# Performance work log

Measured on AMD Instinct MI355X. Metric: run time of the kernel, lower is better.

## Reference

```python
import jax, jax.numpy as jnp
import numpy as np

N, E = 40000, 640000
S_IN, V_IN = 64, 32            # input irreps: 64x0e + 32x1o (dim 160)
S_MID, V_MID = 96, 128         # tp output: (64+32)x0e, (64+32+32)x1o
S_OUT, V_OUT = 96, 32          # gate irreps_in: 64x0e scalars + 32x0e gates + 32x1o gated
R = 64                         # edge scalar (radial basis) dim
FC_HID = 64
W_NUMEL = 64 + 64 + 32 + 32 + 32  # per-edge tp weights ('uvu', v=1): 224
NUM_NEIGHBORS = 16.0


def setup_inputs() -> dict:
    key = jax.random.key(0)
    ks = jax.random.split(key, 13)
    return {
        "node_features": jax.random.normal(ks[0], (N, S_IN + 3 * V_IN), jnp.float32),
        "node_attr": jnp.ones((N, 1), jnp.float32),
        "edge_src": jax.random.randint(ks[1], (E,), 0, N),
        "edge_dst": jax.random.randint(ks[2], (E,), 0, N),
        "edge_attr": jax.random.normal(ks[3], (E, 4), jnp.float32),
        "edge_scalars": jax.random.normal(ks[4], (E, R), jnp.float32),
        "lin1_ws": jax.random.normal(ks[5], (S_IN, S_IN), jnp.float32),
        "lin1_wv": jax.random.normal(ks[6], (V_IN, V_IN), jnp.float32),
        "fc_w1": jax.random.normal(ks[7], (R, FC_HID), jnp.float32),
        "fc_w2": jax.random.normal(ks[8], (FC_HID, W_NUMEL), jnp.float32),
        "sc_ws": jax.random.normal(ks[9], (S_IN, S_OUT), jnp.float32),
        "sc_wv": jax.random.normal(ks[10], (V_IN, V_OUT), jnp.float32),
        "lin2_ws": jax.random.normal(ks[11], (S_MID, S_OUT), jnp.float32),
        "lin2_wv": jax.random.normal(ks[12], (V_MID, V_OUT), jnp.float32),
    }


def _inv(d):
    return 1.0 / jnp.sqrt(jnp.float32(d))


def _forward(node_features, node_attr, edge_attr, edge_scalars,
             lin1_ws, lin1_wv, fc_w1, fc_w2, sc_ws, sc_wv, lin2_ws, lin2_wv,
             edge_src, edge_dst):
    n = node_features.shape[0]
    s = node_features[:, :S_IN]                      # [N,64] 0e
    v = node_features[:, S_IN:].reshape(n, V_IN, 3)  # [N,32,3] 1o
    a = node_attr                                    # [N,1] scalar node attr

    # self-connection: FullyConnectedTensorProduct(input, 1x0e attr, out) == per-irrep linear
    sc_s = (s @ sc_ws) * a * _inv(S_IN)                                    # [N,96]
    sc_v = jnp.einsum('nci,cd->ndi', v, sc_wv) * a[:, :, None] * _inv(V_IN)  # [N,32,3]

    # lin1
    h_s = (s @ lin1_ws) * a * _inv(S_IN)
    h_v = jnp.einsum('nci,cd->ndi', v, lin1_wv) * a[:, :, None] * _inv(V_IN)

    # per-edge tensor-product weights from FC on edge scalars (silu MLP, no bias)
    hid = jax.nn.silu((edge_scalars @ fc_w1) * _inv(R))
    w = (hid @ fc_w2) * _inv(FC_HID)                 # [E,224]
    w1, w2, w3, w4, w5 = jnp.split(w, [64, 128, 160, 192], axis=-1)

    # gather source node features
    es = h_s[edge_src]                               # [E,64]
    ev = h_v[edge_src]                               # [E,32,3]
    e0 = edge_attr[:, :1]                            # [E,1]  0e
    e1 = edge_attr[:, 1:4]                           # [E,3]  1o

    # Clebsch-Gordan tensor product paths ('uvu', per-edge weights)
    m_s1 = w1 * es * e0                                                   # 0e x 0e -> 0e [E,64]
    m_s2 = w4 * jnp.einsum('eci,ei->ec', ev, e1) * _inv(3)                # 1o x 1o -> 0e [E,32]
    m_v1 = (w2 * es)[:, :, None] * e1[:, None, :]                         # 0e x 1o -> 1o [E,64,3]
    m_v2 = w3[:, :, None] * ev * e0[:, :, None]                           # 1o x 0e -> 1o [E,32,3]
    m_v3 = w5[:, :, None] * jnp.cross(ev, e1[:, None, :]) * _inv(2)       # 1o x 1o -> 1o [E,32,3]

    mid_s = jnp.concatenate([m_s1, m_s2], axis=-1)        # [E,96]
    mid_v = jnp.concatenate([m_v1, m_v2, m_v3], axis=1)   # [E,128,3]

    # scatter-sum to destination nodes, normalized by sqrt(num_neighbors)
    inv_nn = 1.0 / jnp.sqrt(jnp.float32(NUM_NEIGHBORS))
    agg_s = jax.ops.segment_sum(mid_s, edge_dst, num_segments=n) * inv_nn
    agg_v = jax.ops.segment_sum(mid_v, edge_dst, num_segments=n) * inv_nn

    # lin2
    o_s = (agg_s @ lin2_ws) * a * _inv(S_MID)                                  # [N,96]
    o_v = jnp.einsum('nci,cd->ndi', agg_v, lin2_wv) * a[:, :, None] * _inv(V_MID)  # [N,32,3]

    pre_s = sc_s + o_s
    pre_v = sc_v + o_v

    # Gate: silu on scalars, sigmoid gates multiply the l=1 features
    scalars = jax.nn.silu(pre_s[:, :64])
    gates = jax.nn.sigmoid(pre_s[:, 64:96])
    gated = gates[:, :, None] * pre_v                 # [N,32,3]
    return jnp.concatenate([scalars, gated.reshape(n, 3 * V_OUT)], axis=-1)  # [N,160]


def reference(node_features, node_attr, edge_src, edge_dst, edge_attr, edge_scalars,
              lin1_ws, lin1_wv, fc_w1, fc_w2, sc_ws, sc_wv, lin2_ws, lin2_wv):
    return _forward(node_features, node_attr, edge_attr, edge_scalars,
                    lin1_ws, lin1_wv, fc_w1, fc_w2, sc_ws, sc_wv, lin2_ws, lin2_wv,
                    edge_src, edge_dst)
```

## Files before the change

kernel.cpp:

```cpp
#include <hip/hip_runtime.h>

constexpr int N_NODES = 40000;
constexpr int N_EDGES = 640000;

constexpr float C_INV8     = 0.125f;
constexpr float C_INV_S32  = 0.17677669529663687f;
constexpr float C_INV_S3   = 0.57735026918962576f;
constexpr float C_INV_S2   = 0.70710678118654752f;
constexpr float C_INV_S96  = 0.10206207261596575f;
constexpr float C_INV_S128 = 0.08838834764831845f;
constexpr float C_INV_NN   = 0.25f;

typedef __attribute__((ext_vector_type(8))) short short8;
typedef __attribute__((ext_vector_type(4))) float f32x4;

__device__ __forceinline__ unsigned short f2bf(float x) {
  __bf16 b = (__bf16)x;
  return __builtin_bit_cast(unsigned short, b);
}
__device__ __forceinline__ float bf2f(unsigned short h) {
  return __uint_as_float(((unsigned int)h) << 16);
}

__global__ __launch_bounds__(256) void k_prep(
    const float* __restrict__ fc_w1, const float* __restrict__ fc_w2,
    const float* __restrict__ lin2_ws, const float* __restrict__ lin2_wv,
    unsigned short* __restrict__ w1t, unsigned short* __restrict__ w2t,
    unsigned short* __restrict__ wst, unsigned short* __restrict__ wvt)
{
  int t = blockIdx.x * 256 + threadIdx.x;
  if (t < 4096) {
    int c = t >> 6, k = t & 63;
    w1t[c * 64 + k] = f2bf(fc_w1[k * 64 + c]);
  } else if (t < 4096 + 14336) {
    int u = t - 4096; int c = u >> 6, k = u & 63;
    w2t[c * 64 + k] = f2bf(fc_w2[k * 224 + c]);
  } else if (t < 18432 + 9216) {
    int u = t - 18432; int c = u / 96, k = u - c * 96;
    wst[c * 96 + k] = f2bf(lin2_ws[k * 96 + c] * (C_INV_NN * C_INV_S96));
  } else if (t < 27648 + 4096) {
    int u = t - 27648; int d = u >> 7, k = u & 127;
    wvt[d * 128 + k] = f2bf(lin2_wv[k * 32 + d] * (C_INV_NN * C_INV_S128));
  }
}

__global__ __launch_bounds__(256) void k_node(
    const float* __restrict__ nf, const float* __restrict__ attr,
    const float* __restrict__ ws_, const float* __restrict__ wv_,
    float* __restrict__ h_s, float* __restrict__ h_v)
{
  int t = blockIdx.x * 256 + threadIdx.x;
  if (t < N_NODES * 64) {
    int n = t >> 6, c = t & 63;
    const float* s = nf + (long)n * 160;
    float acc = 0.f;
    #pragma unroll 8
    for (int k = 0; k < 64; ++k) acc = fmaf(s[k], ws_[k * 64 + c], acc);
    h_s[t] = acc * attr[n] * C_INV8;
  } else {
    int u = t - N_NODES * 64;
    if (u >= N_NODES * 32) return;
    int n = u >> 5, d = u & 31;
    const float* v = nf + (long)n * 160 + 64;
    float a0 = 0.f, a1 = 0.f, a2 = 0.f;
    #pragma unroll 8
    for (int c = 0; c < 32; ++c) {
      float wv = wv_[c * 32 + d];
      a0 = fmaf(v[3 * c + 0], wv, a0);
      a1 = fmaf(v[3 * c + 1], wv, a1);
      a2 = fmaf(v[3 * c + 2], wv, a2);
    }
    float sc = attr[n] * C_INV_S32;
    h_v[(long)u * 3 + 0] = a0 * sc;
    h_v[(long)u * 3 + 1] = a1 * sc;
    h_v[(long)u * 3 + 2] = a2 * sc;
  }
}

__global__ __launch_bounds__(256) void k_deg(const int* __restrict__ edst,
                                             int* __restrict__ deg)
{
  int e = blockIdx.x * 256 + threadIdx.x;
  if (e < N_EDGES) atomicAdd(&deg[edst[e]], 1);
}

__global__ __launch_bounds__(1024) void k_scan(const int* __restrict__ deg,
                                               int* __restrict__ start,
                                               int* __restrict__ cursor)
{
  __shared__ int psum[1024];
  int tid = threadIdx.x;
  const int PER = 40;
  int base = tid * PER;
  int s = 0;
  for (int i = 0; i < PER; ++i) {
    int idx = base + i;
    if (idx < N_NODES) s += deg[idx];
  }
  psum[tid] = s;
  __syncthreads();
  for (int off = 1; off < 1024; off <<= 1) {
    int v = psum[tid];
    int u = (tid >= off) ? psum[tid - off] : 0;
    __syncthreads();
    psum[tid] = v + u;
    __syncthreads();
  }
  int run = (tid == 0) ? 0 : psum[tid - 1];
  for (int i = 0; i < PER; ++i) {
    int idx = base + i;
    if (idx < N_NODES) {
      start[idx] = run; cursor[idx] = run;
      run += deg[idx];
    }
  }
  if (tid == 1023) start[N_NODES] = run;
}

__global__ __launch_bounds__(256) void k_fill(const int* __restrict__ edst,
                                              int* __restrict__ cursor,
                                              int* __restrict__ pos)
{
  int e = blockIdx.x * 256 + threadIdx.x;
  if (e < N_EDGES) {
    int p = atomicAdd(&cursor[edst[e]], 1);
    pos[e] = p;
  }
}

__global__ __launch_bounds__(256, 3) void k_edge2(
    const float* __restrict__ escal, const float* __restrict__ eattr,
    const int* __restrict__ esrc, const int* __restrict__ pos,
    const unsigned short* __restrict__ w1t, const unsigned short* __restrict__ w2t,
    const unsigned short* __restrict__ wst, const unsigned short* __restrict__ wvt,
    const float* __restrict__ h_s, const float* __restrict__ h_v,
    unsigned short* __restrict__ e_out)
{
  __shared__ unsigned short w_lds[64 * 232];
  int tid = threadIdx.x, warp = tid >> 6, lane = tid & 63;
  int lr = lane & 15, lg = lane >> 4;
  long e0 = (long)blockIdx.x * 64;
  int r0 = warp * 16;
  unsigned short* wp = w_lds + r0 * 232;

  long eM = e0 + r0 + lr;
  int srcM = esrc[eM];
  float4 ea4 = *reinterpret_cast<const float4*>(eattr + eM * 4);
  float ea0 = ea4.x, e1x = ea4.y, e1y = ea4.z, e1z = ea4.w;
  float esv[16];
  {
    const float* hsr = h_s + (long)srcM * 64;
    *reinterpret_cast<float4*>(&esv[0])  = *reinterpret_cast<const float4*>(hsr + lg * 8);
    *reinterpret_cast<float4*>(&esv[4])  = *reinterpret_cast<const float4*>(hsr + lg * 8 + 4);
    *reinterpret_cast<float4*>(&esv[8])  = *reinterpret_cast<const float4*>(hsr + 32 + lg * 8);
    *reinterpret_cast<float4*>(&esv[12]) = *reinterpret_cast<const float4*>(hsr + 32 + lg * 8 + 4);
  }
  float evv[24];
  {
    const float* hvr = h_v + (long)srcM * 96 + lg * 24;
    #pragma unroll
    for (int q = 0; q < 6; ++q)
      *reinterpret_cast<float4*>(&evv[4 * q]) = *reinterpret_cast<const float4*>(hvr + 4 * q);
  }

  f32x4 acc[4] = {};
  #pragma unroll
  for (int ks = 0; ks < 2; ++ks) {
    const float* ap = escal + eM * 64 + ks * 32 + lg * 8;
    float4 a01 = *reinterpret_cast<const float4*>(ap);
    float4 a23 = *reinterpret_cast<const float4*>(ap + 4);
    short8 af;
    af[0] = (short)f2bf(a01.x); af[1] = (short)f2bf(a01.y);
    af[2] = (short)f2bf(a01.z); af[3] = (short)f2bf(a01.w);
    af[4] = (short)f2bf(a23.x); af[5] = (short)f2bf(a23.y);
    af[6] = (short)f2bf(a23.z); af[7] = (short)f2bf(a23.w);
    #pragma unroll
    for (int nt = 0; nt < 4; ++nt) {
      short8 bf = *reinterpret_cast<const short8*>(w1t + (nt * 16 + lr) * 64 + ks * 32 + lg * 8);
      acc[nt] = __builtin_amdgcn_mfma_f32_16x16x32_bf16(af, bf, acc[nt], 0, 0, 0);
    }
  }
  #pragma unroll
  for (int nt = 0; nt < 4; ++nt)
    #pragma unroll
    for (int r = 0; r < 4; ++r) {
      float x = acc[nt][r] * C_INV8;
      float h = x / (1.f + __expf(-x));
      wp[(lg * 4 + r) * 72 + nt * 16 + lr] = f2bf(h);
    }

  f32x4 acc2[14] = {};
  #pragma unroll
  for (int ks = 0; ks < 2; ++ks) {
    short8 af = *reinterpret_cast<const short8*>(wp + lr * 72 + ks * 32 + lg * 8);
    #pragma unroll
    for (int nt = 0; nt < 14; ++nt) {
      short8 bf = *reinterpret_cast<const short8*>(w2t + (nt * 16 + lr) * 64 + ks * 32 + lg * 8);
      acc2[nt] = __builtin_amdgcn_mfma_f32_16x16x32_bf16(af, bf, acc2[nt], 0, 0, 0);
    }
  }
  #pragma unroll
  for (int nt = 0; nt < 14; ++nt)
    #pragma unroll
    for (int r = 0; r < 4; ++r)
      wp[(lg * 4 + r) * 232 + nt * 16 + lr] = f2bf(acc2[nt][r] * C_INV8);

  const unsigned short* wrow = wp + lr * 232;
  short8 w1a = *reinterpret_cast<const short8*>(wrow + lg * 8);
  short8 w1b = *reinterpret_cast<const short8*>(wrow + 32 + lg * 8);
  short8 w2a = *reinterpret_cast<const short8*>(wrow + 64 + lg * 8);
  short8 w2b = *reinterpret_cast<const short8*>(wrow + 96 + lg * 8);
  short8 w3s = *reinterpret_cast<const short8*>(wrow + 128 + lg * 8);
  short8 w4s = *reinterpret_cast<const short8*>(wrow + 160 + lg * 8);
  short8 w5s = *reinterpret_cast<const short8*>(wrow + 192 + lg * 8);

  f32x4 accS[6] = {};
  {
    short8 aS;
    #pragma unroll
    for (int j = 0; j < 8; ++j) aS[j] = (short)f2bf(bf2f((unsigned short)w1a[j]) * esv[j] * ea0);
    #pragma unroll
    for (int nt = 0; nt < 6; ++nt) {
      short8 b = *reinterpret_cast<const short8*>(wst + (nt * 16 + lr) * 96 + lg * 8);
      accS[nt] = __builtin_amdgcn_mfma_f32_16x16x32_bf16(aS, b, accS[nt], 0, 0, 0);
    }
    #pragma unroll
    for (int j = 0; j < 8; ++j) aS[j] = (short)f2bf(bf2f((unsigned short)w1b[j]) * esv[8 + j] * ea0);
    #pragma unroll
    for (int nt = 0; nt < 6; ++nt) {
      short8 b = *reinterpret_cast<const short8*>(wst + (nt * 16 + lr) * 96 + 32 + lg * 8);
      accS[nt] = __builtin_amdgcn_mfma_f32_16x16x32_bf16(aS, b, accS[nt], 0, 0, 0);
    }
    #pragma unroll
    for (int j = 0; j < 8; ++j) {
      float dot = evv[3 * j] * e1x + evv[3 * j + 1] * e1y + evv[3 * j + 2] * e1z;
      aS[j] = (short)f2bf(bf2f((unsigned short)w4s[j]) * dot * C_INV_S3);
    }
    #pragma unroll
    for (int nt = 0; nt < 6; ++nt) {
      short8 b = *reinterpret_cast<const short8*>(wst + (nt * 16 + lr) * 96 + 64 + lg * 8);
      accS[nt] = __builtin_amdgcn_mfma_f32_16x16x32_bf16(aS, b, accS[nt], 0, 0, 0);
    }
  }

  f32x4 accV[6] = {};
  #pragma unroll
  for (int i = 0; i < 3; ++i) {
    float e1i = (i == 0) ? e1x : (i == 1) ? e1y : e1z;
    short8 aV;
    #pragma unroll
    for (int j = 0; j < 8; ++j) aV[j] = (short)f2bf(bf2f((unsigned short)w2a[j]) * esv[j] * e1i);
    #pragma unroll
    for (int nt = 0; nt < 2; ++nt) {
      short8 b = *reinterpret_cast<const short8*>(wvt + (nt * 16 + lr) * 128 + lg * 8);
      accV[i * 2 + nt] = __builtin_amdgcn_mfma_f32_16x16x32_bf16(aV, b, accV[i * 2 + nt], 0, 0, 0);
    }
    #pragma unroll
    for (int j = 0; j < 8; ++j) aV[j] = (short)f2bf(bf2f((unsigned short)w2b[j]) * esv[8 + j] * e1i);
    #pragma unroll
    for (int nt = 0; nt < 2; ++nt) {
      short8 b = *reinterpret_cast<const short8*>(wvt + (nt * 16 + lr) * 128 + 32 + lg * 8);
      accV[i * 2 + nt] = __builtin_amdgcn_mfma_f32_16x16x32_bf16(aV, b, accV[i * 2 + nt], 0, 0, 0);
    }
    #pragma unroll
    for (int j = 0; j < 8; ++j) aV[j] = (short)f2bf(bf2f((unsigned short)w3s[j]) * evv[3 * j + i] * ea0);
    #pragma unroll
    for (int nt = 0; nt < 2; ++nt) {
      short8 b = *reinterpret_cast<const short8*>(wvt + (nt * 16 + lr) * 128 + 64 + lg * 8);
      accV[i * 2 + nt] = __builtin_amdgcn_mfma_f32_16x16x32_bf16(aV, b, accV[i * 2 + nt], 0, 0, 0);
    }
    #pragma unroll
    for (int j = 0; j < 8; ++j) {
      float ex = evv[3 * j], ey = evv[3 * j + 1], ez = evv[3 * j + 2];
      float cr = (i == 0) ? (ey * e1z - ez * e1y)
               : (i == 1) ? (ez * e1x - ex * e1z)
                          : (ex * e1y - ey * e1x);
      aV[j] = (short)f2bf(bf2f((unsigned short)w5s[j]) * cr * C_INV_S2);
    }
    #pragma unroll
    for (int nt = 0; nt < 2; ++nt) {
      short8 b = *reinterpret_cast<const short8*>(wvt + (nt * 16 + lr) * 128 + 96 + lg * 8);
      accV[i * 2 + nt] = __builtin_amdgcn_mfma_f32_16x16x32_bf16(aV, b, accV[i * 2 + nt], 0, 0, 0);
    }
  }

  #pragma unroll
  for (int nt = 0; nt < 6; ++nt)
    #pragma unroll
    for (int r = 0; r < 4; ++r)
      wp[(lg * 4 + r) * 232 + nt * 16 + lr] = f2bf(accS[nt][r]);
  #pragma unroll
  for (int q = 0; q < 6; ++q) {
    int i = q >> 1, nt = q & 1;
    #pragma unroll
    for (int r = 0; r < 4; ++r)
      wp[(lg * 4 + r) * 232 + 96 + i * 32 + nt * 16 + lr] = f2bf(accV[q][r]);
  }

  #pragma unroll
  for (int c3 = 0; c3 < 6; ++c3) {
    int chunk = c3 * 64 + lane;
    int row = chunk / 24, col = chunk % 24;
    int p = pos[e0 + r0 + row];
    float4 v4 = *reinterpret_cast<const float4*>(wp + row * 232 + col * 8);
    *reinterpret_cast<float4*>(e_out + (long)p * 192 + col * 8) = v4;
  }
}

__global__ __launch_bounds__(256) void k_agg(
    const int* __restrict__ start, const unsigned short* __restrict__ eo,
    float* __restrict__ agg)
{
  int t = blockIdx.x * 256 + threadIdx.x;
  if (t >= N_NODES * 96) return;
  int n = t / 96, c = t - n * 96;
  int s0 = start[n], s1 = start[n + 1];
  const unsigned int* base = reinterpret_cast<const unsigned int*>(eo);
  float a0 = 0.f, a1 = 0.f;
  long idx = (long)s0 * 96 + c;
  int k = s0;
  for (; k + 8 <= s1; k += 8) {
    unsigned int v[8];
    #pragma unroll
    for (int j = 0; j < 8; ++j) v[j] = base[idx + (long)j * 96];
    #pragma unroll
    for (int j = 0; j < 8; ++j) {
      a0 += bf2f((unsigned short)(v[j] & 0xffffu));
      a1 += bf2f((unsigned short)(v[j] >> 16));
    }
    idx += 8 * 96;
  }
  for (; k < s1; ++k) {
    unsigned int v = base[idx];
    a0 += bf2f((unsigned short)(v & 0xffffu));
    a1 += bf2f((unsigned short)(v >> 16));
    idx += 96;
  }
  agg[(long)n * 192 + 2 * c]     = a0;
  agg[(long)n * 192 + 2 * c + 1] = a1;
}

__global__ __launch_bounds__(256) void k_fin(
    const float* __restrict__ nf, const float* __restrict__ attr,
    const float* __restrict__ agg, const float* __restrict__ sc_ws,
    const float* __restrict__ sc_wv, float* __restrict__ out)
{
  int t = blockIdx.x * 256 + threadIdx.x;
  if (t < N_NODES * 64) {
    int n = t >> 6, cch = t & 63;
    const float* s = nf + (long)n * 160;
    float acc2 = 0.f;
    #pragma unroll 8
    for (int k = 0; k < 64; ++k) acc2 = fmaf(s[k], sc_ws[k * 96 + cch], acc2);
    float pre = (agg[(long)n * 192 + cch] + acc2 * C_INV8) * attr[n];
    out[(long)n * 160 + cch] = pre / (1.f + __expf(-pre));
  } else {
    int u = t - N_NODES * 64;
    if (u >= N_NODES * 32) return;
    int n = u >> 5, d = u & 31;
    const float* s = nf + (long)n * 160;
    float a = attr[n];
    float gacc = 0.f;
    #pragma unroll 8
    for (int k = 0; k < 64; ++k) gacc = fmaf(s[k], sc_ws[k * 96 + 64 + d], gacc);
    float gpre = (agg[(long)n * 192 + 64 + d] + gacc * C_INV8) * a;
    float g = 1.f / (1.f + __expf(-gpre));
    const float* v = s + 64;
    float s0 = 0.f, s1 = 0.f, s2 = 0.f;
    #pragma unroll 8
    for (int cc = 0; cc < 32; ++cc) {
      float wv = sc_wv[cc * 32 + d];
      s0 = fmaf(v[3 * cc + 0], wv, s0);
      s1 = fmaf(v[3 * cc + 1], wv, s1);
      s2 = fmaf(v[3 * cc + 2], wv, s2);
    }
    const float* ag = agg + (long)n * 192 + 96;
    float p0 = (ag[d]      + s0 * C_INV_S32) * a;
    float p1 = (ag[32 + d] + s1 * C_INV_S32) * a;
    float p2 = (ag[64 + d] + s2 * C_INV_S32) * a;
    float* o = out + (long)n * 160 + 64 + 3 * d;
    o[0] = g * p0; o[1] = g * p1; o[2] = g * p2;
  }
}

extern "C" void kernel_launch(void* const* d_in, const int* in_sizes, int n_in,
                              void* d_out, int out_size, void* d_ws, size_t ws_size,
                              hipStream_t stream)
{
  const float* nf      = (const float*)d_in[0];
  const float* attr    = (const float*)d_in[1];
  const int*   esrc    = (const int*)d_in[2];
  const int*   edst    = (const int*)d_in[3];
  const float* eattr   = (const float*)d_in[4];
  const float* escal   = (const float*)d_in[5];
  const float* lin1_ws = (const float*)d_in[6];
  const float* lin1_wv = (const float*)d_in[7];
  const float* fc_w1   = (const float*)d_in[8];
  const float* fc_w2   = (const float*)d_in[9];
  const float* sc_ws   = (const float*)d_in[10];
  const float* sc_wv   = (const float*)d_in[11];
  const float* lin2_ws = (const float*)d_in[12];
  const float* lin2_wv = (const float*)d_in[13];
  float* out = (float*)d_out;

  char* base = (char*)d_ws;
  size_t off = 0;
  auto carve = [&](size_t bytes) { void* p = base + off; off = (off + bytes + 63) & ~(size_t)63; return p; };
  float* h_s   = (float*)carve((size_t)N_NODES * 64 * 4);
  float* h_v   = (float*)carve((size_t)N_NODES * 96 * 4);
  float* agg   = (float*)carve((size_t)N_NODES * 192 * 4);
  unsigned short* w1t = (unsigned short*)carve(4096 * 2);
  unsigned short* w2t = (unsigned short*)carve(14336 * 2);
  unsigned short* wst = (unsigned short*)carve(9216 * 2);
  unsigned short* wvt = (unsigned short*)carve(4096 * 2);
  int* deg    = (int*)carve((size_t)N_NODES * 4);
  int* startp = (int*)carve((size_t)(N_NODES + 1) * 4);
  int* cursor = (int*)carve((size_t)N_NODES * 4);
  int* pos    = (int*)carve((size_t)N_EDGES * 4);
  unsigned short* e_out = (unsigned short*)carve((size_t)N_EDGES * 192 * 2);

  k_prep<<<124, 256, 0, stream>>>(fc_w1, fc_w2, lin2_ws, lin2_wv, w1t, w2t, wst, wvt);
  k_node<<<(N_NODES * 96 + 255) / 256, 256, 0, stream>>>(nf, attr, lin1_ws, lin1_wv, h_s, h_v);

  hipMemsetAsync(deg, 0, (size_t)N_NODES * 4, stream);
  k_deg<<<(N_EDGES + 255) / 256, 256, 0, stream>>>(edst, deg);
  k_scan<<<1, 1024, 0, stream>>>(deg, startp, cursor);
  k_fill<<<(N_EDGES + 255) / 256, 256, 0, stream>>>(edst, cursor, pos);
  k_edge2<<<N_EDGES / 64, 256, 0, stream>>>(escal, eattr, esrc, pos,
                                            w1t, w2t, wst, wvt, h_s, h_v, e_out);
  k_agg<<<(N_NODES * 96 + 255) / 256, 256, 0, stream>>>(startp, e_out, agg);
  k_fin<<<(N_NODES * 96 + 255) / 256, 256, 0, stream>>>(nf, attr, agg, sc_ws, sc_wv, out);
}
```

Before: 698.9 us.

## Fuse node prep with weight prep, fuse aggregation with gate finish

Merges the weight-transpose kernel and the node linear kernel into one launch split by block index. Also fuses the segment aggregation with the self-connection/gate epilogue: each 192-thread block handles two nodes, keeps the aggregated values in shared memory, and no longer writes or reads the fp32 agg buffer. It also drops the occupancy hint of 3 on the edge kernel's launch bounds, which may change register allocation and occupancy there. The fused epilogue keeps roughly the same per-thread work, now with smaller blocks.

```diff
diff --git a/kernel.cpp b/kernel.cpp
--- a/kernel.cpp
+++ b/kernel.cpp
@@ -22,58 +22,60 @@
   return __uint_as_float(((unsigned int)h) << 16);
 }
 
-__global__ __launch_bounds__(256) void k_prep(
+constexpr int NODE_BLOCKS = (N_NODES * 96 + 255) / 256;
+constexpr int PREP_BLOCKS = 124;
+
+__global__ __launch_bounds__(256) void k_pre(
+    const float* __restrict__ nf, const float* __restrict__ attr,
+    const float* __restrict__ ws_, const float* __restrict__ wv_,
     const float* __restrict__ fc_w1, const float* __restrict__ fc_w2,
     const float* __restrict__ lin2_ws, const float* __restrict__ lin2_wv,
+    float* __restrict__ h_s, float* __restrict__ h_v,
     unsigned short* __restrict__ w1t, unsigned short* __restrict__ w2t,
     unsigned short* __restrict__ wst, unsigned short* __restrict__ wvt)
 {
-  int t = blockIdx.x * 256 + threadIdx.x;
-  if (t < 4096) {
-    int c = t >> 6, k = t & 63;
-    w1t[c * 64 + k] = f2bf(fc_w1[k * 64 + c]);
-  } else if (t < 4096 + 14336) {
-    int u = t - 4096; int c = u >> 6, k = u & 63;
-    w2t[c * 64 + k] = f2bf(fc_w2[k * 224 + c]);
-  } else if (t < 18432 + 9216) {
-    int u = t - 18432; int c = u / 96, k = u - c * 96;
-    wst[c * 96 + k] = f2bf(lin2_ws[k * 96 + c] * (C_INV_NN * C_INV_S96));
-  } else if (t < 27648 + 4096) {
-    int u = t - 27648; int d = u >> 7, k = u & 127;
-    wvt[d * 128 + k] = f2bf(lin2_wv[k * 32 + d] * (C_INV_NN * C_INV_S128));
-  }
-}
-
-__global__ __launch_bounds__(256) void k_node(
-    const float* __restrict__ nf, const float* __restrict__ attr,
-    const float* __restrict__ ws_, const float* __restrict__ wv_,
-    float* __restrict__ h_s, float* __restrict__ h_v)
-{
-  int t = blockIdx.x * 256 + threadIdx.x;
-  if (t < N_NODES * 64) {
-    int n = t >> 6, c = t & 63;
-    const float* s = nf + (long)n * 160;
-    float acc = 0.f;
-    #pragma unroll 8
-    for (int k = 0; k < 64; ++k) acc = fmaf(s[k], ws_[k * 64 + c], acc);
-    h_s[t] = acc * attr[n] * C_INV8;
+  if (blockIdx.x < NODE_BLOCKS) {
+    int t = blockIdx.x * 256 + threadIdx.x;
+    if (t < N_NODES * 64) {
+      int n = t >> 6, c = t & 63;
+      const float* s = nf + (long)n * 160;
+      float acc = 0.f;
+      #pragma unroll 8
+      for (int k = 0; k < 64; ++k) acc = fmaf(s[k], ws_[k * 64 + c], acc);
+      h_s[t] = acc * attr[n] * C_INV8;
+    } else {
+      int u = t - N_NODES * 64;
+      if (u >= N_NODES * 32) return;
+      int n = u >> 5, d = u & 31;
+      const float* v = nf + (long)n * 160 + 64;
+      float a0 = 0.f, a1 = 0.f, a2 = 0.f;
+      #pragma unroll 8
+      for (int c = 0; c < 32; ++c) {
+        float wv = wv_[c * 32 + d];
+        a0 = fmaf(v[3 * c + 0], wv, a0);
+        a1 = fmaf(v[3 * c + 1], wv, a1);
+        a2 = fmaf(v[3 * c + 2], wv, a2);
+      }
+      float sc = attr[n] * C_INV_S32;
+      h_v[(long)u * 3 + 0] = a0 * sc;
+      h_v[(long)u * 3 + 1] = a1 * sc;
+      h_v[(long)u * 3 + 2] = a2 * sc;
+    }
   } else {
-    int u = t - N_NODES * 64;
-    if (u >= N_NODES * 32) return;
-    int n = u >> 5, d = u & 31;
-    const float* v = nf + (long)n * 160 + 64;
-    float a0 = 0.f, a1 = 0.f, a2 = 0.f;
-    #pragma unroll 8
-    for (int c = 0; c < 32; ++c) {
-      float wv = wv_[c * 32 + d];
-      a0 = fmaf(v[3 * c + 0], wv, a0);
-      a1 = fmaf(v[3 * c + 1], wv, a1);
-      a2 = fmaf(v[3 * c + 2], wv, a2);
-    }
-    float sc = attr[n] * C_INV_S32;
-    h_v[(long)u * 3 + 0] = a0 * sc;
-    h_v[(long)u * 3 + 1] = a1 * sc;
-    h_v[(long)u * 3 + 2] = a2 * sc;
+    int t = (blockIdx.x - NODE_BLOCKS) * 256 + threadIdx.x;
+    if (t < 4096) {
+      int c = t >> 6, k = t & 63;
+      w1t[c * 64 + k] = f2bf(fc_w1[k * 64 + c]);
+    } else if (t < 4096 + 14336) {
+      int u = t - 4096; int c = u >> 6, k = u & 63;
+      w2t[c * 64 + k] = f2bf(fc_w2[k * 224 + c]);
+    } else if (t < 18432 + 9216) {
+      int u = t - 18432; int c = u / 96, k = u - c * 96;
+      wst[c * 96 + k] = f2bf(lin2_ws[k * 96 + c] * (C_INV_NN * C_INV_S96));
+    } else if (t < 27648 + 4096) {
+      int u = t - 27648; int d = u >> 7, k = u & 127;
+      wvt[d * 128 + k] = f2bf(lin2_wv[k * 32 + d] * (C_INV_NN * C_INV_S128));
+    }
   }
 }
 
@@ -128,7 +130,7 @@
   }
 }
 
-__global__ __launch_bounds__(256, 3) void k_edge2(
+__global__ __launch_bounds__(256) void k_edge2(
     const float* __restrict__ escal, const float* __restrict__ eattr,
     const int* __restrict__ esrc, const int* __restrict__ pos,
     const unsigned short* __restrict__ w1t, const unsigned short* __restrict__ w2t,
@@ -307,13 +309,17 @@
   }
 }
 
-__global__ __launch_bounds__(256) void k_agg(
+__global__ __launch_bounds__(192) void k_aggfin(
     const int* __restrict__ start, const unsigned short* __restrict__ eo,
-    float* __restrict__ agg)
-{
-  int t = blockIdx.x * 256 + threadIdx.x;
-  if (t >= N_NODES * 96) return;
-  int n = t / 96, c = t - n * 96;
+    const float* __restrict__ nf, const float* __restrict__ attr,
+    const float* __restrict__ sc_ws, const float* __restrict__ sc_wv,
+    float* __restrict__ out)
+{
+  __shared__ float sm[2][192];
+  int tid = threadIdx.x;
+  int ln = tid / 96, c = tid - ln * 96;
+  int n = blockIdx.x * 2 + ln;
+
   int s0 = start[n], s1 = start[n + 1];
   const unsigned int* base = reinterpret_cast<const unsigned int*>(eo);
   float a0 = 0.f, a1 = 0.f;
@@ -336,48 +342,38 @@
     a1 += bf2f((unsigned short)(v >> 16));
     idx += 96;
   }
-  agg[(long)n * 192 + 2 * c]     = a0;
-  agg[(long)n * 192 + 2 * c + 1] = a1;
-}
-
-__global__ __launch_bounds__(256) void k_fin(
-    const float* __restrict__ nf, const float* __restrict__ attr,
-    const float* __restrict__ agg, const float* __restrict__ sc_ws,
-    const float* __restrict__ sc_wv, float* __restrict__ out)
-{
-  int t = blockIdx.x * 256 + threadIdx.x;
-  if (t < N_NODES * 64) {
-    int n = t >> 6, cch = t & 63;
-    const float* s = nf + (long)n * 160;
+  sm[ln][2 * c]     = a0;
+  sm[ln][2 * c + 1] = a1;
+  __syncthreads();
+
+  const float* s = nf + (long)n * 160;
+  float a = attr[n];
+  if (c < 64) {
     float acc2 = 0.f;
     #pragma unroll 8
-    for (int k = 0; k < 64; ++k) acc2 = fmaf(s[k], sc_ws[k * 96 + cch], acc2);
-    float pre = (agg[(long)n * 192 + cch] + acc2 * C_INV8) * attr[n];
-    out[(long)n * 160 + cch] = pre / (1.f + __expf(-pre));
+    for (int kk = 0; kk < 64; ++kk) acc2 = fmaf(s[kk], sc_ws[kk * 96 + c], acc2);
+    float pre = (sm[ln][c] + acc2 * C_INV8) * a;
+    out[(long)n * 160 + c] = pre / (1.f + __expf(-pre));
   } else {
-    int u = t - N_NODES * 64;
-    if (u >= N_NODES * 32) return;
-    int n = u >> 5, d = u & 31;
-    const float* s = nf + (long)n * 160;
-    float a = attr[n];
+    int d = c - 64;
     float gacc = 0.f;
     #pragma unroll 8
-    for (int k = 0; k < 64; ++k) gacc = fmaf(s[k], sc_ws[k * 96 + 64 + d], gacc);
-    float gpre = (agg[(long)n * 192 + 64 + d] + gacc * C_INV8) * a;
+    for (int kk = 0; kk < 64; ++kk) gacc = fmaf(s[kk], sc_ws[kk * 96 + 64 + d], gacc);
+    float gpre = (sm[ln][64 + d] + gacc * C_INV8) * a;
     float g = 1.f / (1.f + __expf(-gpre));
     const float* v = s + 64;
-    float s0 = 0.f, s1 = 0.f, s2 = 0.f;
+    float s0v = 0.f, s1v = 0.f, s2v = 0.f;
     #pragma unroll 8
     for (int cc = 0; cc < 32; ++cc) {
       float wv = sc_wv[cc * 32 + d];
-      s0 = fmaf(v[3 * cc + 0], wv, s0);
-      s1 = fmaf(v[3 * cc + 1], wv, s1);
-      s2 = fmaf(v[3 * cc + 2], wv, s2);
-    }
-    const float* ag = agg + (long)n * 192 + 96;
-    float p0 = (ag[d]      + s0 * C_INV_S32) * a;
-    float p1 = (ag[32 + d] + s1 * C_INV_S32) * a;
-    float p2 = (ag[64 + d] + s2 * C_INV_S32) * a;
+      s0v = fmaf(v[3 * cc + 0], wv, s0v);
+      s1v = fmaf(v[3 * cc + 1], wv, s1v);
+      s2v = fmaf(v[3 * cc + 2], wv, s2v);
+    }
+    const float* ag = sm[ln] + 96;
+    float p0 = (ag[d]      + s0v * C_INV_S32) * a;
+    float p1 = (ag[32 + d] + s1v * C_INV_S32) * a;
+    float p2 = (ag[64 + d] + s2v * C_INV_S32) * a;
     float* o = out + (long)n * 160 + 64 + 3 * d;
     o[0] = g * p0; o[1] = g * p1; o[2] = g * p2;
   }
@@ -408,7 +404,6 @@
   auto carve = [&](size_t bytes) { void* p = base + off; off = (off + bytes + 63) & ~(size_t)63; return p; };
   float* h_s   = (float*)carve((size_t)N_NODES * 64 * 4);
   float* h_v   = (float*)carve((size_t)N_NODES * 96 * 4);
-  float* agg   = (float*)carve((size_t)N_NODES * 192 * 4);
   unsigned short* w1t = (unsigned short*)carve(4096 * 2);
   unsigned short* w2t = (unsigned short*)carve(14336 * 2);
   unsigned short* wst = (unsigned short*)carve(9216 * 2);
@@ -419,8 +414,9 @@
   int* pos    = (int*)carve((size_t)N_EDGES * 4);
   unsigned short* e_out = (unsigned short*)carve((size_t)N_EDGES * 192 * 2);
 
-  k_prep<<<124, 256, 0, stream>>>(fc_w1, fc_w2, lin2_ws, lin2_wv, w1t, w2t, wst, wvt);
-  k_node<<<(N_NODES * 96 + 255) / 256, 256, 0, stream>>>(nf, attr, lin1_ws, lin1_wv, h_s, h_v);
+  k_pre<<<NODE_BLOCKS + PREP_BLOCKS, 256, 0, stream>>>(
+      nf, attr, lin1_ws, lin1_wv, fc_w1, fc_w2, lin2_ws, lin2_wv,
+      h_s, h_v, w1t, w2t, wst, wvt);
 
   hipMemsetAsync(deg, 0, (size_t)N_NODES * 4, stream);
   k_deg<<<(N_EDGES + 255) / 256, 256, 0, stream>>>(edst, deg);
@@ -428,6 +424,6 @@
   k_fill<<<(N_EDGES + 255) / 256, 256, 0, stream>>>(edst, cursor, pos);
   k_edge2<<<N_EDGES / 64, 256, 0, stream>>>(escal, eattr, esrc, pos,
                                             w1t, w2t, wst, wvt, h_s, h_v, e_out);
-  k_agg<<<(N_NODES * 96 + 255) / 256, 256, 0, stream>>>(startp, e_out, agg);
-  k_fin<<<(N_NODES * 96 + 255) / 256, 256, 0, stream>>>(nf, attr, agg, sc_ws, sc_wv, out);
-}
+  k_aggfin<<<N_NODES / 2, 192, 0, stream>>>(startp, e_out, nf, attr,
+                                            sc_ws, sc_wv, out);
+}
```

Measured after the change: 752.0 us. +7.6%, slower.
